# Kernel optimization log

Hardware: AMD Instinct MI355X
Metric: run time of the kernel (lower is better)

The kernel has to match this reference:

```python
import jax, jax.numpy as jnp
import numpy as np

BATCH, SEQ, IN_DIM, HID, OUT = 256, 512, 256, 1024, 128


def setup_inputs() -> dict:
    key = jax.random.key(0)
    ks = jax.random.split(key, 6)
    s_in = 1.0 / np.sqrt(IN_DIM)
    s_h = 1.0 / np.sqrt(HID)
    return {
        "x": jax.random.normal(ks[0], (BATCH, SEQ, IN_DIM), dtype=jnp.float32),
        "W_hx": jax.random.uniform(ks[1], (HID, IN_DIM), minval=-s_in, maxval=s_in, dtype=jnp.float32),
        "b_hx": jax.random.uniform(ks[2], (HID,), minval=-s_in, maxval=s_in, dtype=jnp.float32),
        "W_hh": jax.random.uniform(ks[3], (HID, HID), minval=-s_h, maxval=s_h, dtype=jnp.float32),
        "W_ho": jax.random.uniform(ks[4], (OUT, HID), minval=-s_h, maxval=s_h, dtype=jnp.float32),
        "b_ho": jax.random.uniform(ks[5], (OUT,), minval=-s_h, maxval=s_h, dtype=jnp.float32),
    }


def reference(x, W_hx, b_hx, W_hh, W_ho, b_ho):
    # Precompute input projections for all timesteps in one big GEMM: [B,S,H]
    xproj = jnp.einsum("bsi,hi->bsh", x, W_hx) + b_hx
    h0 = jnp.zeros((x.shape[0], W_hh.shape[0]), dtype=x.dtype)

    def step(h, xp_t):
        h_new = jnp.tanh(xp_t + h @ W_hh.T)
        return h_new, None

    h_last, _ = jax.lax.scan(step, h0, jnp.swapaxes(xproj, 0, 1))  # scan over time
    logits = h_last @ W_ho.T + b_ho
    return jax.nn.softmax(logits, axis=-1)
```

## Files before the change

kernel.cpp:

```cpp
#include <hip/hip_runtime.h>


typedef __attribute__((ext_vector_type(8))) short short8;
typedef __attribute__((ext_vector_type(4))) float f32x4;
typedef __attribute__((ext_vector_type(4))) unsigned short u16x4;
typedef unsigned short u16;
typedef unsigned long long u64;

#define MF(A, B, C) (C) = __builtin_amdgcn_mfma_f32_16x16x32_bf16((A), (B), (C), 0, 0, 0)

#define XPACK_OFF   0UL
#define WPACK_OFF   67108864UL
#define WHOP_OFF    69730304UL
#define HGLOB_OFF   69992448UL
#define FLAGS_OFF   71041024UL

__device__ __forceinline__ u16 f2bf(float f) {
  union { float f; unsigned u; } v; v.f = f;
  unsigned r = v.u + 0x7FFFu + ((v.u >> 16) & 1u);
  return (u16)(r >> 16);
}

__device__ __forceinline__ float tanh_fast(float x) {
  float cx = fminf(10.f, fmaxf(-10.f, x));
  float e = __expf(2.f * cx);
  return (e - 1.f) / (e + 1.f);
}

__global__ __launch_bounds__(256) void zero_flags_kernel(int* __restrict__ f) {
  f[blockIdx.x * 256 + threadIdx.x] = 0;
}

__global__ __launch_bounds__(256) void pack_x_kernel(const float* __restrict__ x, u16* __restrict__ xpack) {
  const int l = threadIdx.x & 63;
  const int rib = threadIdx.x >> 6;
  const long bt = (long)blockIdx.x * 4 + rib;
  const int b = (int)(bt >> 9);
  const int t = (int)(bt & 511);
  const f32x4 xv = *(const f32x4*)(x + bt * 256 + l * 4);
  const int k = l * 4;
  const int g = b >> 4;
  const int c = k >> 5;
  const int lt = ((k >> 3) & 3) * 16 + (b & 15);
  const int j = k & 7;
  u16x4 o;
  o[0] = f2bf(xv[0]); o[1] = f2bf(xv[1]); o[2] = f2bf(xv[2]); o[3] = f2bf(xv[3]);
  const long idx = ((((long)g * 512 + t) * 8 + c) * 64 + lt) * 8 + j;
  *(u16x4*)(xpack + idx) = o;
}

__global__ __launch_bounds__(256) void pack_w_kernel(const float* __restrict__ Whh, const float* __restrict__ Whx,
                                                     const float* __restrict__ Who, u16* __restrict__ wpack,
                                                     u16* __restrict__ whop) {
  const int fid = blockIdx.x * 256 + threadIdx.x;
  const int l = fid & 63;
  const int frag = fid >> 6;
  const float* src;
  u16* dst;
  if (frag < 2560) {
    const int nt = frag & 3;
    const int kc = (frag >> 2) % 10;
    const int sw = frag / 40;
    const int w = sw & 3, s = sw >> 2;
    const int n = s * 64 + nt * 16 + (l & 15);
    if (kc < 8) src = Whh + n * 1024 + 32 * (8 * w + kc) + 8 * (l >> 4);
    else        src = Whx + n * 256  + 32 * (2 * w + kc - 8) + 8 * (l >> 4);
    dst = wpack + ((long)frag * 64 + l) * 8;
  } else if (frag < 2816) {
    const int f2 = frag - 2560;
    const int c = f2 & 31, nt = f2 >> 5;
    const int o = nt * 16 + (l & 15);
    src = Who + o * 1024 + 32 * c + 8 * (l >> 4);
    dst = whop + ((long)f2 * 64 + l) * 8;
  } else {
    return;
  }
  const f32x4 a = *(const f32x4*)src;
  const f32x4 b = *(const f32x4*)(src + 4);
  u16x4 o0, o1;
  o0[0] = f2bf(a[0]); o0[1] = f2bf(a[1]); o0[2] = f2bf(a[2]); o0[3] = f2bf(a[3]);
  o1[0] = f2bf(b[0]); o1[1] = f2bf(b[1]); o1[2] = f2bf(b[2]); o1[3] = f2bf(b[3]);
  *(u16x4*)dst = o0;
  *(u16x4*)(dst + 4) = o1;
}

extern "C" __global__ __launch_bounds__(256, 1) void rnn_main(
    const short8* __restrict__ xpack, const short8* __restrict__ wpack,
    const short8* __restrict__ whop, const float* __restrict__ bhx,
    const float* __restrict__ bho, u16* __restrict__ hglob,
    int* __restrict__ flags, float* __restrict__ out) {
  __shared__ f32x4 red_lds[16 * 64];
  extern __shared__ f32x4 red2[];

  const int tid = threadIdx.x;
  const int w = tid >> 6;
  const int l = tid & 63;
  const int lr = l & 15, lgp = l >> 4;
  const int bid = blockIdx.x;
  const int g = bid & 15;
  const int s = bid >> 4;

  short8 wreg[10][4];
  {
    const short8* wp = wpack + (long)(s * 4 + w) * 10 * 4 * 64;
#pragma unroll
    for (int kc = 0; kc < 10; kc++)
#pragma unroll
      for (int nt = 0; nt < 4; nt++)
        wreg[kc][nt] = wp[(kc * 4 + nt) * 64 + l];
  }
  const float bias = bhx[s * 64 + w * 16 + lr];
  const int n = s * 64 + w * 16 + lr;
  const int cst = n >> 5, ltb = ((n >> 3) & 3) * 16, jst = n & 7;

#pragma unroll 1
  for (int t = 0; t < 512; ++t) {
    const short8* xp = xpack + (long)(g * 512 + t) * 8 * 64;
    short8 xa0 = xp[(2 * w + 0) * 64 + l];
    short8 xa1 = xp[(2 * w + 1) * 64 + l];

    f32x4 acc0 = {0.f, 0.f, 0.f, 0.f};
    f32x4 acc1 = acc0, acc2 = acc0, acc3 = acc0;

    MF(xa0, wreg[8][0], acc0); MF(xa0, wreg[8][1], acc1);
    MF(xa0, wreg[8][2], acc2); MF(xa0, wreg[8][3], acc3);
    MF(xa1, wreg[9][0], acc0); MF(xa1, wreg[9][1], acc1);
    MF(xa1, wreg[9][2], acc2); MF(xa1, wreg[9][3], acc3);

    if (t > 0) {
      const int* fp = flags + (size_t)((t - 1) * 16 + g) * 32;
      int v = __hip_atomic_load(fp, __ATOMIC_RELAXED, __HIP_MEMORY_SCOPE_AGENT);
      while (v < 16) {
        __builtin_amdgcn_s_sleep(1);
        v = __hip_atomic_load(fp, __ATOMIC_RELAXED, __HIP_MEMORY_SCOPE_AGENT);
      }
      unsigned dep = 0;
      asm volatile("" : "+v"(dep) : "v"(v));
      const u64* hq = (const u64*)(hglob + (size_t)(g * 2 + (t & 1)) * 16384) + dep;
      short8 ha[8];
#pragma unroll
      for (int i = 0; i < 8; i++) {
        union { u64 q[2]; short8 v8; } hu;
        const size_t qi = ((size_t)(w * 8 + i) * 64 + l) * 2;
        hu.q[0] = __hip_atomic_load(hq + qi + 0, __ATOMIC_RELAXED, __HIP_MEMORY_SCOPE_AGENT);
        hu.q[1] = __hip_atomic_load(hq + qi + 1, __ATOMIC_RELAXED, __HIP_MEMORY_SCOPE_AGENT);
        ha[i] = hu.v8;
      }
#pragma unroll
      for (int i = 0; i < 8; i++) {
        MF(ha[i], wreg[i][0], acc0);
        MF(ha[i], wreg[i][1], acc1);
        MF(ha[i], wreg[i][2], acc2);
        MF(ha[i], wreg[i][3], acc3);
      }
    }

    red_lds[(w * 4 + 0) * 64 + l] = acc0;
    red_lds[(w * 4 + 1) * 64 + l] = acc1;
    red_lds[(w * 4 + 2) * 64 + l] = acc2;
    red_lds[(w * 4 + 3) * 64 + l] = acc3;
    __syncthreads();
    f32x4 ssum = red_lds[(0 + w) * 64 + l] + red_lds[(4 + w) * 64 + l] +
                 red_lds[(8 + w) * 64 + l] + red_lds[(12 + w) * 64 + l];

    u16* dst = hglob + (size_t)(g * 2 + ((t + 1) & 1)) * 16384;
#pragma unroll
    for (int r = 0; r < 4; r++) {
      float hv = tanh_fast(ssum[r] + bias);
      __hip_atomic_store(dst + (size_t)(cst * 64 + ltb + 4 * lgp + r) * 8 + jst,
                         f2bf(hv), __ATOMIC_RELAXED, __HIP_MEMORY_SCOPE_AGENT);
    }
    __builtin_amdgcn_fence(__ATOMIC_RELEASE, "workgroup");
    __syncthreads();
    if (tid == 0)
      __hip_atomic_fetch_add(flags + (size_t)(t * 16 + g) * 32, 1,
                             __ATOMIC_RELAXED, __HIP_MEMORY_SCOPE_AGENT);
  }

  if (s != 0) return;
  {
    const int* fp = flags + (size_t)(511 * 16 + g) * 32;
    int v = __hip_atomic_load(fp, __ATOMIC_RELAXED, __HIP_MEMORY_SCOPE_AGENT);
    while (v < 16) {
      __builtin_amdgcn_s_sleep(1);
      v = __hip_atomic_load(fp, __ATOMIC_RELAXED, __HIP_MEMORY_SCOPE_AGENT);
    }
    unsigned dep = 0;
    asm volatile("" : "+v"(dep) : "v"(v));
    const u64* hq = (const u64*)(hglob + (size_t)(g * 2 + 0) * 16384) + dep;
    f32x4 oa[8] = {};
#pragma unroll
    for (int i = 0; i < 8; i++) {
      union { u64 q[2]; short8 v8; } hu;
      const size_t qi = ((size_t)(w * 8 + i) * 64 + l) * 2;
      hu.q[0] = __hip_atomic_load(hq + qi + 0, __ATOMIC_RELAXED, __HIP_MEMORY_SCOPE_AGENT);
      hu.q[1] = __hip_atomic_load(hq + qi + 1, __ATOMIC_RELAXED, __HIP_MEMORY_SCOPE_AGENT);
      short8 ha = hu.v8;
#pragma unroll
      for (int nt = 0; nt < 8; nt++)
        MF(ha, whop[(nt * 32 + w * 8 + i) * 64 + l], oa[nt]);
    }
#pragma unroll
    for (int nt = 0; nt < 8; nt++) red2[(w * 8 + nt) * 64 + l] = oa[nt];
  }
  __syncthreads();
#pragma unroll
  for (int q = 0; q < 2; q++) {
    const int nt = 2 * w + q;
    f32x4 lq = red2[(0 + nt) * 64 + l] + red2[(8 + nt) * 64 + l] +
               red2[(16 + nt) * 64 + l] + red2[(24 + nt) * 64 + l];
    const float bo = bho[nt * 16 + lr];
    lq[0] += bo; lq[1] += bo; lq[2] += bo; lq[3] += bo;
    red_lds[nt * 64 + l] = lq;
  }
  __syncthreads();
  if (w == 0) {
    const int b = l >> 2, q = l & 3;
    const float* redf = (const float*)red_lds;
    float vv[32];
    float mx = -3.0e38f;
#pragma unroll
    for (int jj = 0; jj < 32; jj++) {
      const int o = q * 32 + jj;
      const int nt = o >> 4, m = o & 15;
      const float lv = redf[(nt * 64 + (b >> 2) * 16 + m) * 4 + (b & 3)];
      vv[jj] = lv;
      mx = fmaxf(mx, lv);
    }
    mx = fmaxf(mx, __shfl_xor(mx, 1));
    mx = fmaxf(mx, __shfl_xor(mx, 2));
    float se = 0.f;
#pragma unroll
    for (int jj = 0; jj < 32; jj++) { float e = __expf(vv[jj] - mx); vv[jj] = e; se += e; }
    se += __shfl_xor(se, 1);
    se += __shfl_xor(se, 2);
    const float inv = 1.f / se;
#pragma unroll
    for (int jj = 0; jj < 32; jj++)
      out[(g * 16 + b) * 128 + q * 32 + jj] = vv[jj] * inv;
  }
}

extern "C" void kernel_launch(void* const* d_in, const int* in_sizes, int n_in,
                              void* d_out, int out_size, void* d_ws, size_t ws_size,
                              hipStream_t stream) {
  const float* x   = (const float*)d_in[0];
  const float* Whx = (const float*)d_in[1];
  const float* bhx = (const float*)d_in[2];
  const float* Whh = (const float*)d_in[3];
  const float* Who = (const float*)d_in[4];
  const float* bho = (const float*)d_in[5];
  float* out = (float*)d_out;
  char* ws = (char*)d_ws;

  u16* xpack = (u16*)(ws + XPACK_OFF);
  u16* wpack = (u16*)(ws + WPACK_OFF);
  u16* whop  = (u16*)(ws + WHOP_OFF);
  u16* hglob = (u16*)(ws + HGLOB_OFF);
  int* flags = (int*)(ws + FLAGS_OFF);

  zero_flags_kernel<<<1024, 256, 0, stream>>>(flags);
  pack_x_kernel<<<32768, 256, 0, stream>>>(x, xpack);
  pack_w_kernel<<<704, 256, 0, stream>>>(Whh, Whx, Who, wpack, whop);

  size_t dynsz = 73728;
  if (hipFuncSetAttribute((const void*)rnn_main,
                          hipFuncAttributeMaxDynamicSharedMemorySize, 73728) != hipSuccess)
    dynsz = 49152;

  rnn_main<<<256, 256, dynsz, stream>>>((const short8*)xpack, (const short8*)wpack,
                                        (const short8*)whop, bhx, bho, hglob, flags, out);
}
```

Measured before the change: 1.296 ms.

## Signal per-wave completion flags, double-buffer reduction LDS, prefetch next x tile

Drops the second per-step workgroup barrier and release fence. Each wave now waits for its own global stores (s_waitcnt vmcnt(0)) and increments the step flag itself, so consumers wait for a count of 64 instead of 16. The reduction LDS buffer is double-buffered so that skipping the barrier cannot race with the next step's writes. The next timestep's x fragments are also prefetched into registers one iteration ahead. Dynamic shared memory is reduced to keep total LDS within budget, and the change relies on relaxed agent-scope ordering between the data stores and the flag increment.

```diff
diff --git a/kernel.cpp b/kernel.cpp
--- a/kernel.cpp
+++ b/kernel.cpp
@@ -5,9 +5,12 @@
 typedef __attribute__((ext_vector_type(4))) float f32x4;
 typedef __attribute__((ext_vector_type(4))) unsigned short u16x4;
 typedef unsigned short u16;
+typedef unsigned int u32;
 typedef unsigned long long u64;
 
 #define MF(A, B, C) (C) = __builtin_amdgcn_mfma_f32_16x16x32_bf16((A), (B), (C), 0, 0, 0)
+#define ALOAD(p)    __hip_atomic_load((p), __ATOMIC_RELAXED, __HIP_MEMORY_SCOPE_AGENT)
+#define ASTORE(p,v) __hip_atomic_store((p), (v), __ATOMIC_RELAXED, __HIP_MEMORY_SCOPE_AGENT)
 
 #define XPACK_OFF   0UL
 #define WPACK_OFF   67108864UL
@@ -89,7 +92,7 @@
     const short8* __restrict__ whop, const float* __restrict__ bhx,
     const float* __restrict__ bho, u16* __restrict__ hglob,
     int* __restrict__ flags, float* __restrict__ out) {
-  __shared__ f32x4 red_lds[16 * 64];
+  __shared__ f32x4 red_lds[2][16 * 64];
   extern __shared__ f32x4 red2[];
 
   const int tid = threadIdx.x;
@@ -113,11 +116,22 @@
   const int n = s * 64 + w * 16 + lr;
   const int cst = n >> 5, ltb = ((n >> 3) & 3) * 16, jst = n & 7;
 
+  short8 nxa0, nxa1;
+  {
+    const short8* xp0 = xpack + (long)(g * 512 + 0) * 8 * 64;
+    nxa0 = xp0[(2 * w + 0) * 64 + l];
+    nxa1 = xp0[(2 * w + 1) * 64 + l];
+  }
+
 #pragma unroll 1
   for (int t = 0; t < 512; ++t) {
-    const short8* xp = xpack + (long)(g * 512 + t) * 8 * 64;
-    short8 xa0 = xp[(2 * w + 0) * 64 + l];
-    short8 xa1 = xp[(2 * w + 1) * 64 + l];
+    short8 xa0 = nxa0, xa1 = nxa1;
+    {
+      const int tn = (t + 1) & 511;
+      const short8* xpn = xpack + (long)(g * 512 + tn) * 8 * 64;
+      nxa0 = xpn[(2 * w + 0) * 64 + l];
+      nxa1 = xpn[(2 * w + 1) * 64 + l];
+    }
 
     f32x4 acc0 = {0.f, 0.f, 0.f, 0.f};
     f32x4 acc1 = acc0, acc2 = acc0, acc3 = acc0;
@@ -129,10 +143,10 @@
 
     if (t > 0) {
       const int* fp = flags + (size_t)((t - 1) * 16 + g) * 32;
-      int v = __hip_atomic_load(fp, __ATOMIC_RELAXED, __HIP_MEMORY_SCOPE_AGENT);
-      while (v < 16) {
+      int v = ALOAD(fp);
+      while (v < 64) {
         __builtin_amdgcn_s_sleep(1);
-        v = __hip_atomic_load(fp, __ATOMIC_RELAXED, __HIP_MEMORY_SCOPE_AGENT);
+        v = ALOAD(fp);
       }
       unsigned dep = 0;
       asm volatile("" : "+v"(dep) : "v"(v));
@@ -142,8 +156,8 @@
       for (int i = 0; i < 8; i++) {
         union { u64 q[2]; short8 v8; } hu;
         const size_t qi = ((size_t)(w * 8 + i) * 64 + l) * 2;
-        hu.q[0] = __hip_atomic_load(hq + qi + 0, __ATOMIC_RELAXED, __HIP_MEMORY_SCOPE_AGENT);
-        hu.q[1] = __hip_atomic_load(hq + qi + 1, __ATOMIC_RELAXED, __HIP_MEMORY_SCOPE_AGENT);
+        hu.q[0] = ALOAD(hq + qi + 0);
+        hu.q[1] = ALOAD(hq + qi + 1);
         ha[i] = hu.v8;
       }
 #pragma unroll
@@ -155,24 +169,23 @@
       }
     }
 
-    red_lds[(w * 4 + 0) * 64 + l] = acc0;
-    red_lds[(w * 4 + 1) * 64 + l] = acc1;
-    red_lds[(w * 4 + 2) * 64 + l] = acc2;
-    red_lds[(w * 4 + 3) * 64 + l] = acc3;
+    f32x4* red = red_lds[t & 1];
+    red[(w * 4 + 0) * 64 + l] = acc0;
+    red[(w * 4 + 1) * 64 + l] = acc1;
+    red[(w * 4 + 2) * 64 + l] = acc2;
+    red[(w * 4 + 3) * 64 + l] = acc3;
     __syncthreads();
-    f32x4 ssum = red_lds[(0 + w) * 64 + l] + red_lds[(4 + w) * 64 + l] +
-                 red_lds[(8 + w) * 64 + l] + red_lds[(12 + w) * 64 + l];
+    f32x4 ssum = red[(0 + w) * 64 + l] + red[(4 + w) * 64 + l] +
+                 red[(8 + w) * 64 + l] + red[(12 + w) * 64 + l];
 
     u16* dst = hglob + (size_t)(g * 2 + ((t + 1) & 1)) * 16384;
 #pragma unroll
     for (int r = 0; r < 4; r++) {
       float hv = tanh_fast(ssum[r] + bias);
-      __hip_atomic_store(dst + (size_t)(cst * 64 + ltb + 4 * lgp + r) * 8 + jst,
-                         f2bf(hv), __ATOMIC_RELAXED, __HIP_MEMORY_SCOPE_AGENT);
-    }
-    __builtin_amdgcn_fence(__ATOMIC_RELEASE, "workgroup");
-    __syncthreads();
-    if (tid == 0)
+      ASTORE(dst + (size_t)(cst * 64 + ltb + 4 * lgp + r) * 8 + jst, f2bf(hv));
+    }
+    asm volatile("s_waitcnt vmcnt(0)" ::: "memory");
+    if (l == 0)
       __hip_atomic_fetch_add(flags + (size_t)(t * 16 + g) * 32, 1,
                              __ATOMIC_RELAXED, __HIP_MEMORY_SCOPE_AGENT);
   }
@@ -180,10 +193,10 @@
   if (s != 0) return;
   {
     const int* fp = flags + (size_t)(511 * 16 + g) * 32;
-    int v = __hip_atomic_load(fp, __ATOMIC_RELAXED, __HIP_MEMORY_SCOPE_AGENT);
-    while (v < 16) {
+    int v = ALOAD(fp);
+    while (v < 64) {
       __builtin_amdgcn_s_sleep(1);
-      v = __hip_atomic_load(fp, __ATOMIC_RELAXED, __HIP_MEMORY_SCOPE_AGENT);
+      v = ALOAD(fp);
     }
     unsigned dep = 0;
     asm volatile("" : "+v"(dep) : "v"(v));
@@ -193,8 +206,8 @@
     for (int i = 0; i < 8; i++) {
       union { u64 q[2]; short8 v8; } hu;
       const size_t qi = ((size_t)(w * 8 + i) * 64 + l) * 2;
-      hu.q[0] = __hip_atomic_load(hq + qi + 0, __ATOMIC_RELAXED, __HIP_MEMORY_SCOPE_AGENT);
-      hu.q[1] = __hip_atomic_load(hq + qi + 1, __ATOMIC_RELAXED, __HIP_MEMORY_SCOPE_AGENT);
+      hu.q[0] = ALOAD(hq + qi + 0);
+      hu.q[1] = ALOAD(hq + qi + 1);
       short8 ha = hu.v8;
 #pragma unroll
       for (int nt = 0; nt < 8; nt++)
@@ -205,23 +218,23 @@
   }
   __syncthreads();
 #pragma unroll
-  for (int q = 0; q < 2; q++) {
-    const int nt = 2 * w + q;
+  for (int qd = 0; qd < 2; qd++) {
+    const int nt = 2 * w + qd;
     f32x4 lq = red2[(0 + nt) * 64 + l] + red2[(8 + nt) * 64 + l] +
                red2[(16 + nt) * 64 + l] + red2[(24 + nt) * 64 + l];
     const float bo = bho[nt * 16 + lr];
     lq[0] += bo; lq[1] += bo; lq[2] += bo; lq[3] += bo;
-    red_lds[nt * 64 + l] = lq;
+    red_lds[0][nt * 64 + l] = lq;
   }
   __syncthreads();
   if (w == 0) {
-    const int b = l >> 2, q = l & 3;
-    const float* redf = (const float*)red_lds;
+    const int b = l >> 2, qd = l & 3;
+    const float* redf = (const float*)red_lds[0];
     float vv[32];
     float mx = -3.0e38f;
 #pragma unroll
     for (int jj = 0; jj < 32; jj++) {
-      const int o = q * 32 + jj;
+      const int o = qd * 32 + jj;
       const int nt = o >> 4, m = o & 15;
       const float lv = redf[(nt * 64 + (b >> 2) * 16 + m) * 4 + (b & 3)];
       vv[jj] = lv;
@@ -237,7 +250,7 @@
     const float inv = 1.f / se;
 #pragma unroll
     for (int jj = 0; jj < 32; jj++)
-      out[(g * 16 + b) * 128 + q * 32 + jj] = vv[jj] * inv;
+      out[(g * 16 + b) * 128 + qd * 32 + jj] = vv[jj] * inv;
   }
 }
 
@@ -263,10 +276,10 @@
   pack_x_kernel<<<32768, 256, 0, stream>>>(x, xpack);
   pack_w_kernel<<<704, 256, 0, stream>>>(Whh, Whx, Who, wpack, whop);
 
-  size_t dynsz = 73728;
+  size_t dynsz = 57344;
   if (hipFuncSetAttribute((const void*)rnn_main,
-                          hipFuncAttributeMaxDynamicSharedMemorySize, 73728) != hipSuccess)
-    dynsz = 49152;
+                          hipFuncAttributeMaxDynamicSharedMemorySize, 57344) != hipSuccess)
+    dynsz = 32768;
 
   rnn_main<<<256, 256, dynsz, stream>>>((const short8*)xpack, (const short8*)wpack,
                                         (const short8*)whop, bhx, bho, hglob, flags, out);
```

Measured after the change: 1.966 ms. 51.7% more time.

## Split per-step flags by slice group and widen h stores via swapped MFMA operands

Applied to the files above, without the earlier changes.

The per-timestep completion counter per batch group is split into four counters, one per group of four slices, so each wave waits only on the producers of the hidden chunk it reads, and only lane 0 polls. MFMA operands are swapped so each lane holds four consecutive hidden units, which lets the tanh output be written as one 64-bit atomic store instead of four 16-bit ones. Bias and the softmax indexing are adjusted to the transposed layout. This adds a larger flag array and finer-grained dependencies, but it means less contention on one counter and fewer store transactions per step.

```diff
diff --git a/kernel.cpp b/kernel.cpp
--- a/kernel.cpp
+++ b/kernel.cpp
@@ -5,9 +5,12 @@
 typedef __attribute__((ext_vector_type(4))) float f32x4;
 typedef __attribute__((ext_vector_type(4))) unsigned short u16x4;
 typedef unsigned short u16;
+typedef unsigned int u32;
 typedef unsigned long long u64;
 
 #define MF(A, B, C) (C) = __builtin_amdgcn_mfma_f32_16x16x32_bf16((A), (B), (C), 0, 0, 0)
+#define ALOAD(p)    __hip_atomic_load((p), __ATOMIC_RELAXED, __HIP_MEMORY_SCOPE_AGENT)
+#define ASTORE(p,v) __hip_atomic_store((p), (v), __ATOMIC_RELAXED, __HIP_MEMORY_SCOPE_AGENT)
 
 #define XPACK_OFF   0UL
 #define WPACK_OFF   67108864UL
@@ -28,7 +31,7 @@
 }
 
 __global__ __launch_bounds__(256) void zero_flags_kernel(int* __restrict__ f) {
-  f[blockIdx.x * 256 + threadIdx.x] = 0;
+  f[(size_t)blockIdx.x * 256 + threadIdx.x] = 0;
 }
 
 __global__ __launch_bounds__(256) void pack_x_kernel(const float* __restrict__ x, u16* __restrict__ xpack) {
@@ -102,16 +105,17 @@
 
   short8 wreg[10][4];
   {
-    const short8* wp = wpack + (long)(s * 4 + w) * 10 * 4 * 64;
+    const short8* wp = wpack + (long)(s * 4 + w) * 40 * 64;
 #pragma unroll
     for (int kc = 0; kc < 10; kc++)
 #pragma unroll
       for (int nt = 0; nt < 4; nt++)
         wreg[kc][nt] = wp[(kc * 4 + nt) * 64 + l];
   }
-  const float bias = bhx[s * 64 + w * 16 + lr];
-  const int n = s * 64 + w * 16 + lr;
-  const int cst = n >> 5, ltb = ((n >> 3) & 3) * 16, jst = n & 7;
+  const int n0 = s * 64 + w * 16 + 4 * lgp;
+  const f32x4 biasv = *(const f32x4*)(bhx + n0);
+  const int hc = n0 >> 5, hq = (n0 >> 3) & 3, hj = n0 & 7;
+  const size_t hoff = (size_t)((hc * 64 + hq * 16 + lr) * 8 + hj);
 
 #pragma unroll 1
   for (int t = 0; t < 512; ++t) {
@@ -122,36 +126,35 @@
     f32x4 acc0 = {0.f, 0.f, 0.f, 0.f};
     f32x4 acc1 = acc0, acc2 = acc0, acc3 = acc0;
 
-    MF(xa0, wreg[8][0], acc0); MF(xa0, wreg[8][1], acc1);
-    MF(xa0, wreg[8][2], acc2); MF(xa0, wreg[8][3], acc3);
-    MF(xa1, wreg[9][0], acc0); MF(xa1, wreg[9][1], acc1);
-    MF(xa1, wreg[9][2], acc2); MF(xa1, wreg[9][3], acc3);
+    MF(wreg[8][0], xa0, acc0); MF(wreg[8][1], xa0, acc1);
+    MF(wreg[8][2], xa0, acc2); MF(wreg[8][3], xa0, acc3);
+    MF(wreg[9][0], xa1, acc0); MF(wreg[9][1], xa1, acc1);
+    MF(wreg[9][2], xa1, acc2); MF(wreg[9][3], xa1, acc3);
 
     if (t > 0) {
-      const int* fp = flags + (size_t)((t - 1) * 16 + g) * 32;
-      int v = __hip_atomic_load(fp, __ATOMIC_RELAXED, __HIP_MEMORY_SCOPE_AGENT);
-      while (v < 16) {
-        __builtin_amdgcn_s_sleep(1);
-        v = __hip_atomic_load(fp, __ATOMIC_RELAXED, __HIP_MEMORY_SCOPE_AGENT);
+      const int* fq = flags + (((size_t)(t - 1) * 16 + g) * 4 + w) * 32;
+      if (l == 0) {
+        while (ALOAD(fq) < 4) __builtin_amdgcn_s_sleep(1);
       }
+      int v = (l == 0) ? 1 : 0;
       unsigned dep = 0;
       asm volatile("" : "+v"(dep) : "v"(v));
-      const u64* hq = (const u64*)(hglob + (size_t)(g * 2 + (t & 1)) * 16384) + dep;
+      const u64* hq8 = (const u64*)(hglob + (size_t)(g * 2 + (t & 1)) * 16384) + dep;
       short8 ha[8];
 #pragma unroll
       for (int i = 0; i < 8; i++) {
         union { u64 q[2]; short8 v8; } hu;
         const size_t qi = ((size_t)(w * 8 + i) * 64 + l) * 2;
-        hu.q[0] = __hip_atomic_load(hq + qi + 0, __ATOMIC_RELAXED, __HIP_MEMORY_SCOPE_AGENT);
-        hu.q[1] = __hip_atomic_load(hq + qi + 1, __ATOMIC_RELAXED, __HIP_MEMORY_SCOPE_AGENT);
+        hu.q[0] = ALOAD(hq8 + qi + 0);
+        hu.q[1] = ALOAD(hq8 + qi + 1);
         ha[i] = hu.v8;
       }
 #pragma unroll
       for (int i = 0; i < 8; i++) {
-        MF(ha[i], wreg[i][0], acc0);
-        MF(ha[i], wreg[i][1], acc1);
-        MF(ha[i], wreg[i][2], acc2);
-        MF(ha[i], wreg[i][3], acc3);
+        MF(wreg[i][0], ha[i], acc0);
+        MF(wreg[i][1], ha[i], acc1);
+        MF(wreg[i][2], ha[i], acc2);
+        MF(wreg[i][3], ha[i], acc3);
       }
     }
 
@@ -164,66 +167,62 @@
                  red_lds[(8 + w) * 64 + l] + red_lds[(12 + w) * 64 + l];
 
     u16* dst = hglob + (size_t)(g * 2 + ((t + 1) & 1)) * 16384;
-#pragma unroll
-    for (int r = 0; r < 4; r++) {
-      float hv = tanh_fast(ssum[r] + bias);
-      __hip_atomic_store(dst + (size_t)(cst * 64 + ltb + 4 * lgp + r) * 8 + jst,
-                         f2bf(hv), __ATOMIC_RELAXED, __HIP_MEMORY_SCOPE_AGENT);
-    }
+    union { u16x4 v; u64 q; } pu;
+#pragma unroll
+    for (int r = 0; r < 4; r++) pu.v[r] = f2bf(tanh_fast(ssum[r] + biasv[r]));
+    ASTORE((u64*)(dst + hoff), pu.q);
     __builtin_amdgcn_fence(__ATOMIC_RELEASE, "workgroup");
     __syncthreads();
     if (tid == 0)
-      __hip_atomic_fetch_add(flags + (size_t)(t * 16 + g) * 32, 1,
+      __hip_atomic_fetch_add(flags + (((size_t)t * 16 + g) * 4 + (s >> 2)) * 32, 1,
                              __ATOMIC_RELAXED, __HIP_MEMORY_SCOPE_AGENT);
   }
 
   if (s != 0) return;
   {
-    const int* fp = flags + (size_t)(511 * 16 + g) * 32;
-    int v = __hip_atomic_load(fp, __ATOMIC_RELAXED, __HIP_MEMORY_SCOPE_AGENT);
-    while (v < 16) {
-      __builtin_amdgcn_s_sleep(1);
-      v = __hip_atomic_load(fp, __ATOMIC_RELAXED, __HIP_MEMORY_SCOPE_AGENT);
-    }
+    const int* fq = flags + (((size_t)511 * 16 + g) * 4 + w) * 32;
+    if (l == 0) {
+      while (ALOAD(fq) < 4) __builtin_amdgcn_s_sleep(1);
+    }
+    int v = (l == 0) ? 1 : 0;
     unsigned dep = 0;
     asm volatile("" : "+v"(dep) : "v"(v));
-    const u64* hq = (const u64*)(hglob + (size_t)(g * 2 + 0) * 16384) + dep;
+    const u64* hq8 = (const u64*)(hglob + (size_t)(g * 2 + 0) * 16384) + dep;
     f32x4 oa[8] = {};
 #pragma unroll
     for (int i = 0; i < 8; i++) {
       union { u64 q[2]; short8 v8; } hu;
       const size_t qi = ((size_t)(w * 8 + i) * 64 + l) * 2;
-      hu.q[0] = __hip_atomic_load(hq + qi + 0, __ATOMIC_RELAXED, __HIP_MEMORY_SCOPE_AGENT);
-      hu.q[1] = __hip_atomic_load(hq + qi + 1, __ATOMIC_RELAXED, __HIP_MEMORY_SCOPE_AGENT);
+      hu.q[0] = ALOAD(hq8 + qi + 0);
+      hu.q[1] = ALOAD(hq8 + qi + 1);
       short8 ha = hu.v8;
 #pragma unroll
       for (int nt = 0; nt < 8; nt++)
-        MF(ha, whop[(nt * 32 + w * 8 + i) * 64 + l], oa[nt]);
+        MF(whop[(nt * 32 + w * 8 + i) * 64 + l], ha, oa[nt]);
     }
 #pragma unroll
     for (int nt = 0; nt < 8; nt++) red2[(w * 8 + nt) * 64 + l] = oa[nt];
   }
   __syncthreads();
 #pragma unroll
-  for (int q = 0; q < 2; q++) {
-    const int nt = 2 * w + q;
+  for (int qd = 0; qd < 2; qd++) {
+    const int nt = 2 * w + qd;
     f32x4 lq = red2[(0 + nt) * 64 + l] + red2[(8 + nt) * 64 + l] +
                red2[(16 + nt) * 64 + l] + red2[(24 + nt) * 64 + l];
-    const float bo = bho[nt * 16 + lr];
-    lq[0] += bo; lq[1] += bo; lq[2] += bo; lq[3] += bo;
+    const f32x4 bov = *(const f32x4*)(bho + nt * 16 + 4 * lgp);
+    lq[0] += bov[0]; lq[1] += bov[1]; lq[2] += bov[2]; lq[3] += bov[3];
     red_lds[nt * 64 + l] = lq;
   }
   __syncthreads();
   if (w == 0) {
-    const int b = l >> 2, q = l & 3;
+    const int b = l >> 2, qd = l & 3;
     const float* redf = (const float*)red_lds;
     float vv[32];
     float mx = -3.0e38f;
 #pragma unroll
     for (int jj = 0; jj < 32; jj++) {
-      const int o = q * 32 + jj;
-      const int nt = o >> 4, m = o & 15;
-      const float lv = redf[(nt * 64 + (b >> 2) * 16 + m) * 4 + (b & 3)];
+      const int o = qd * 32 + jj;
+      const float lv = redf[((o >> 4) * 64 + ((o >> 2) & 3) * 16 + b) * 4 + (o & 3)];
       vv[jj] = lv;
       mx = fmaxf(mx, lv);
     }
@@ -237,7 +236,7 @@
     const float inv = 1.f / se;
 #pragma unroll
     for (int jj = 0; jj < 32; jj++)
-      out[(g * 16 + b) * 128 + q * 32 + jj] = vv[jj] * inv;
+      out[(g * 16 + b) * 128 + qd * 32 + jj] = vv[jj] * inv;
   }
 }
 
@@ -259,7 +258,7 @@
   u16* hglob = (u16*)(ws + HGLOB_OFF);
   int* flags = (int*)(ws + FLAGS_OFF);
 
-  zero_flags_kernel<<<1024, 256, 0, stream>>>(flags);
+  zero_flags_kernel<<<4096, 256, 0, stream>>>(flags);
   pack_x_kernel<<<32768, 256, 0, stream>>>(x, xpack);
   pack_w_kernel<<<704, 256, 0, stream>>>(Whh, Whx, Who, wpack, whop);
 
```

Result: no change. 1.278 ms (-1.4%).
